# Kernel tuning notes

Hardware: AMD Instinct MI355X
Metric: run time of the kernel (lower is better)

Reference implementation:

```python
import jax, jax.numpy as jnp
import numpy as np

LEAK = 0.2
N = 1024      # nodes
C_IN = 64     # input channels
C_OUT = 64    # output channels
L = 2         # num_degrees -> L**2 = 4 spherical-harmonic index
LSQ = L * L
T = 15        # num_eret (edge retyping)


def setup_inputs() -> dict:
    key = jax.random.key(0)
    k1, k2, k3, k4 = jax.random.split(key, 4)
    x = jax.random.normal(k1, (N, C_IN), dtype=jnp.float32)
    adjacency = jax.random.normal(k2, (N, N, LSQ, T), dtype=jnp.float32)
    # learned params (truncated_normal init in keras; plain normal*0.05 here)
    W = jax.random.normal(k3, (C_IN, C_OUT, LSQ, T), dtype=jnp.float32) * 0.05
    W2 = jax.random.normal(k4, (C_IN, C_OUT), dtype=jnp.float32) * 0.05
    return {"x": x, "adjacency": adjacency, "W": W, "W2": W2}


def reference(x, adjacency, W, W2):
    # adjacency-weighted spherical-harmonic message passing:
    # temp[m, j] = sum_{n,i,l,t} adj[m,n,l,t] * x[n,i] * W[i,j,l,t]
    temp = jnp.einsum('mnlt,ni,ijlt->mj', adjacency, x, W)
    # skip / self connection
    temp = temp + jnp.einsum('ni,ij->nj', x, W2)
    # lrelu with leak 0.2 (use_bias=False)
    return jnp.maximum(temp, LEAK * temp)
```

## Files before the change

kernel.cpp:

```cpp
#include <hip/hip_runtime.h>
#include <hip/hip_bf16.h>
#include <stdint.h>

typedef __bf16 v8bf __attribute__((ext_vector_type(8)));
typedef float  v4f  __attribute__((ext_vector_type(4)));

#define LEAK 0.2f

static __device__ __forceinline__ unsigned short bf16rne(float f) {
    union { float f; uint32_t u; } v; v.f = f;
    return (unsigned short)((v.u + 0x7FFFu + ((v.u >> 16) & 1u)) >> 16);
}

static __device__ __forceinline__ void gload16(const void* g, void* l) {
    __builtin_amdgcn_global_load_lds(
        (const __attribute__((address_space(1))) void*)g,
        (__attribute__((address_space(3))) void*)l, 16, 0, 0);
}

__global__ __launch_bounds__(256) void k0_wt(const float* __restrict__ W,
                                             unsigned short* __restrict__ Wt) {
    __shared__ float tile[64][65];
    const int c0 = blockIdx.x * 64;
    const int t  = threadIdx.x;
    {
        const int cl = t & 63, ig = t >> 6;
#pragma unroll
        for (int r = 0; r < 16; ++r) {
            int i = ig + (r << 2);
            tile[i][cl] = W[i * 3840 + c0 + cl];
        }
    }
    __syncthreads();
    {
        const int il = t & 63, cg = t >> 6;
#pragma unroll
        for (int r = 0; r < 16; ++r) {
            int c = cg + (r << 2);
            Wt[(c0 + c) * 64 + il] = bf16rne(tile[il][c]);
        }
    }
}

__global__ __launch_bounds__(256) void k1_ygemm(const float* __restrict__ x,
                                                const unsigned short* __restrict__ Wt,
                                                unsigned short* __restrict__ Yt) {
    __shared__ unsigned short As[64 * 64];
    __shared__ unsigned short Bs[64 * 64];
    const int blk = blockIdx.x;
    const int nt = blk / 60, ct = blk % 60;
    const int n0 = nt * 64, c0 = ct * 64;
    const int t = threadIdx.x;
    char* const asb = (char*)As;
    char* const bsb = (char*)Bs;

#pragma unroll
    for (int r = 0; r < 4; ++r) {
        const int rr = (t >> 4) + (r << 4);
        const int cq = t & 15;
        const float4 v = *reinterpret_cast<const float4*>(x + (n0 + rr) * 64 + cq * 4);
        uint2 p;
        p.x = (uint32_t)bf16rne(v.x) | ((uint32_t)bf16rne(v.y) << 16);
        p.y = (uint32_t)bf16rne(v.z) | ((uint32_t)bf16rne(v.w) << 16);
        const int off = rr * 128 + ((cq * 8) ^ ((rr & 7) << 4));
        *reinterpret_cast<uint2*>(asb + off) = p;
    }
#pragma unroll
    for (int r = 0; r < 2; ++r) {
        const int chunk = t + (r << 8);
        const int row = chunk >> 3, c16 = chunk & 7;
        const uint4 v = *reinterpret_cast<const uint4*>(Wt + (c0 + row) * 64 + c16 * 8);
        const int off = row * 128 + ((c16 * 16) ^ ((row & 7) << 4));
        *reinterpret_cast<uint4*>(bsb + off) = v;
    }
    __syncthreads();

    const int w = t >> 6, l = t & 63;
    v4f acc[4];
#pragma unroll
    for (int jt = 0; jt < 4; ++jt) acc[jt] = (v4f){0.f, 0.f, 0.f, 0.f};

#pragma unroll
    for (int s = 0; s < 2; ++s) {
        const int ar = 16 * w + (l & 15);
        const v8bf af = *reinterpret_cast<const v8bf*>(
            asb + ar * 128 + ((64 * s + (l >> 4) * 16) ^ ((ar & 7) << 4)));
#pragma unroll
        for (int jt = 0; jt < 4; ++jt) {
            const int br = 16 * jt + (l & 15);
            const v8bf bf = *reinterpret_cast<const v8bf*>(
                bsb + br * 128 + ((64 * s + (l >> 4) * 16) ^ ((br & 7) << 4)));
            acc[jt] = __builtin_amdgcn_mfma_f32_16x16x32_bf16(af, bf, acc[jt], 0, 0, 0);
        }
    }

#pragma unroll
    for (int jt = 0; jt < 4; ++jt) {
#pragma unroll
        for (int r = 0; r < 4; ++r) {
            const int n = n0 + 16 * w + (l >> 4) * 4 + r;
            const int c = c0 + jt * 16 + (l & 15);
            const int j = c / 60, lt = c % 60;
            Yt[j * 61440 + n * 60 + lt] = bf16rne(acc[jt][r]);
        }
    }
}

__global__ __launch_bounds__(256) void k2_main(const float* __restrict__ adj,
                                               const unsigned short* __restrict__ Yt,
                                               float* __restrict__ partial) {
    __shared__ __align__(16) char lds[73728];
    const int blk = blockIdx.x;
    const int mt = blk >> 5, ks = blk & 31;
    const int m0 = mt * 64;
    const long kc0 = (long)ks * 1920;
    const int t = threadIdx.x;
    const int w = t >> 6, l = t & 63;
    const int lr = l & 15, lg = l >> 4;

    const char* srcA[4];
    const char* srcB[2];
#pragma unroll
    for (int k = 0; k < 4; ++k) {
        const int row = k * 16 + w * 4 + lg;
        srcA[k] = (const char*)(adj + (size_t)(m0 + row) * 61440 + kc0)
                  + ((lr * 16) ^ ((row & 7) << 4));
    }
#pragma unroll
    for (int k = 0; k < 2; ++k) {
        const int row = k * 32 + w * 8 + (l >> 3);
        srcB[k] = (const char*)(Yt + (size_t)row * 61440 + kc0)
                  + (((l & 7) * 16) ^ ((row & 7) << 4));
    }

#define STAGE(bs, s) do {                                                      \
        char* ab_ = lds + (bs) * 16384;                                        \
        char* bb_ = lds + 49152 + (bs) * 8192;                                 \
        _Pragma("unroll")                                                      \
        for (int k_ = 0; k_ < 4; ++k_)                                         \
            gload16(srcA[k_] + (size_t)(s) * 256, ab_ + k_ * 4096 + w * 1024); \
        _Pragma("unroll")                                                      \
        for (int k_ = 0; k_ < 2; ++k_)                                         \
            gload16(srcB[k_] + (size_t)(s) * 128, bb_ + k_ * 4096 + w * 1024); \
    } while (0)

    v4f acc[4];
#pragma unroll
    for (int jt = 0; jt < 4; ++jt) acc[jt] = (v4f){0.f, 0.f, 0.f, 0.f};

    const int ar = 16 * w + lr;
    const int sa = (ar & 7) << 4;

    STAGE(0, 0);
    STAGE(1, 1);
    int bs = 2, bc = 0;

#pragma unroll 1
    for (int i = 0; i < 30; ++i) {
        if (i < 29) { asm volatile("s_waitcnt vmcnt(6)" ::: "memory"); }
        else        { asm volatile("s_waitcnt vmcnt(0)" ::: "memory"); }
        __builtin_amdgcn_s_barrier();
        asm volatile("" ::: "memory");
        if (i < 28) STAGE(bs, i + 2);

        const char* ab = lds + bc * 16384;
        const char* bb = lds + 49152 + bc * 8192;
        v8bf af[2];
#pragma unroll
        for (int ss = 0; ss < 2; ++ss) {
            const int Xf = ss * 128 + lg * 32;
            const float4 x0 = *reinterpret_cast<const float4*>(ab + ar * 256 + (Xf ^ sa));
            const float4 x1 = *reinterpret_cast<const float4*>(ab + ar * 256 + ((Xf + 16) ^ sa));
            v8bf f;
            f[0] = (__bf16)x0.x; f[1] = (__bf16)x0.y;
            f[2] = (__bf16)x0.z; f[3] = (__bf16)x0.w;
            f[4] = (__bf16)x1.x; f[5] = (__bf16)x1.y;
            f[6] = (__bf16)x1.z; f[7] = (__bf16)x1.w;
            af[ss] = f;
        }
#pragma unroll
        for (int jt = 0; jt < 4; ++jt) {
            const int br = 16 * jt + lr;
            const int sb = (br & 7) << 4;
            const v8bf b0 = *reinterpret_cast<const v8bf*>(bb + br * 128 + ((lg * 16) ^ sb));
            const v8bf b1 = *reinterpret_cast<const v8bf*>(bb + br * 128 + ((64 + lg * 16) ^ sb));
            acc[jt] = __builtin_amdgcn_mfma_f32_16x16x32_bf16(af[0], b0, acc[jt], 0, 0, 0);
            acc[jt] = __builtin_amdgcn_mfma_f32_16x16x32_bf16(af[1], b1, acc[jt], 0, 0, 0);
        }

        bs = (bs == 2) ? 0 : bs + 1;
        bc = (bc == 2) ? 0 : bc + 1;
    }
#undef STAGE

    float* const p = partial + (long)ks * 65536;
#pragma unroll
    for (int jt = 0; jt < 4; ++jt) {
#pragma unroll
        for (int r = 0; r < 4; ++r) {
            const int m = m0 + 16 * w + lg * 4 + r;
            const int j = jt * 16 + lr;
            p[m * 64 + j] = acc[jt][r];
        }
    }
}

__global__ __launch_bounds__(256) void k3_epi(const float* __restrict__ partial,
                                              const float* __restrict__ x,
                                              const float* __restrict__ W2,
                                              float* __restrict__ out) {
    const int idx = blockIdx.x * 256 + threadIdx.x;
    const int m = idx >> 6, j = idx & 63;
    float s = 0.f;
#pragma unroll 8
    for (int sp = 0; sp < 32; ++sp) s += partial[sp * 65536 + idx];
    float sk = 0.f;
#pragma unroll 8
    for (int i = 0; i < 64; ++i) sk += x[m * 64 + i] * W2[i * 64 + j];
    const float v = s + sk;
    out[idx] = fmaxf(v, LEAK * v);
}

extern "C" void kernel_launch(void* const* d_in, const int* in_sizes, int n_in,
                              void* d_out, int out_size, void* d_ws, size_t ws_size,
                              hipStream_t stream) {
    const float* x   = (const float*)d_in[0];
    const float* adj = (const float*)d_in[1];
    const float* W   = (const float*)d_in[2];
    const float* W2  = (const float*)d_in[3];
    float* out = (float*)d_out;

    char* ws = (char*)d_ws;
    unsigned short* Wt = (unsigned short*)ws;
    unsigned short* Yt = (unsigned short*)(ws + 524288);
    float* partial     = (float*)(ws + 8388608);

    k0_wt   <<<60,  256, 0, stream>>>(W, Wt);
    k1_ygemm<<<960, 256, 0, stream>>>(x, Wt, Yt);
    k2_main <<<512, 256, 0, stream>>>(adj, Yt, partial);
    k3_epi  <<<256, 256, 0, stream>>>(partial, x, W2, out);
}
```

Baseline: 59.51 us.

## Fuse W transpose into Y GEMM and split-K reduction into main kernel

Removes the separate W transpose kernel by having the Y GEMM read fp32 W directly from global memory with strided loads and convert it in registers. Removes the epilogue kernel by having the last-arriving block per row tile, found with an atomic counter, reduce the split-K partials and apply the skip GEMM and leaky ReLU. Partials are now stored as bf16 to halve their traffic. This cuts launch count and partial traffic, at the cost of uncoalesced W reads, a memset, a serialized tail on the last block and lower precision in the reduction.

```diff
diff --git a/kernel.cpp b/kernel.cpp
--- a/kernel.cpp
+++ b/kernel.cpp
@@ -11,85 +11,46 @@
     union { float f; uint32_t u; } v; v.f = f;
     return (unsigned short)((v.u + 0x7FFFu + ((v.u >> 16) & 1u)) >> 16);
 }
-
+static __device__ __forceinline__ float bf2f(unsigned short s) {
+    union { uint32_t u; float f; } v; v.u = (uint32_t)s << 16; return v.f;
+}
 static __device__ __forceinline__ void gload16(const void* g, void* l) {
     __builtin_amdgcn_global_load_lds(
         (const __attribute__((address_space(1))) void*)g,
         (__attribute__((address_space(3))) void*)l, 16, 0, 0);
 }
 
-__global__ __launch_bounds__(256) void k0_wt(const float* __restrict__ W,
-                                             unsigned short* __restrict__ Wt) {
-    __shared__ float tile[64][65];
-    const int c0 = blockIdx.x * 64;
-    const int t  = threadIdx.x;
-    {
-        const int cl = t & 63, ig = t >> 6;
-#pragma unroll
-        for (int r = 0; r < 16; ++r) {
-            int i = ig + (r << 2);
-            tile[i][cl] = W[i * 3840 + c0 + cl];
-        }
-    }
-    __syncthreads();
-    {
-        const int il = t & 63, cg = t >> 6;
-#pragma unroll
-        for (int r = 0; r < 16; ++r) {
-            int c = cg + (r << 2);
-            Wt[(c0 + c) * 64 + il] = bf16rne(tile[il][c]);
-        }
-    }
-}
-
 __global__ __launch_bounds__(256) void k1_ygemm(const float* __restrict__ x,
-                                                const unsigned short* __restrict__ Wt,
+                                                const float* __restrict__ W,
                                                 unsigned short* __restrict__ Yt) {
-    __shared__ unsigned short As[64 * 64];
-    __shared__ unsigned short Bs[64 * 64];
     const int blk = blockIdx.x;
     const int nt = blk / 60, ct = blk % 60;
     const int n0 = nt * 64, c0 = ct * 64;
     const int t = threadIdx.x;
-    char* const asb = (char*)As;
-    char* const bsb = (char*)Bs;
-
-#pragma unroll
-    for (int r = 0; r < 4; ++r) {
-        const int rr = (t >> 4) + (r << 4);
-        const int cq = t & 15;
-        const float4 v = *reinterpret_cast<const float4*>(x + (n0 + rr) * 64 + cq * 4);
-        uint2 p;
-        p.x = (uint32_t)bf16rne(v.x) | ((uint32_t)bf16rne(v.y) << 16);
-        p.y = (uint32_t)bf16rne(v.z) | ((uint32_t)bf16rne(v.w) << 16);
-        const int off = rr * 128 + ((cq * 8) ^ ((rr & 7) << 4));
-        *reinterpret_cast<uint2*>(asb + off) = p;
-    }
-#pragma unroll
-    for (int r = 0; r < 2; ++r) {
-        const int chunk = t + (r << 8);
-        const int row = chunk >> 3, c16 = chunk & 7;
-        const uint4 v = *reinterpret_cast<const uint4*>(Wt + (c0 + row) * 64 + c16 * 8);
-        const int off = row * 128 + ((c16 * 16) ^ ((row & 7) << 4));
-        *reinterpret_cast<uint4*>(bsb + off) = v;
-    }
-    __syncthreads();
-
     const int w = t >> 6, l = t & 63;
+    const int lr = l & 15, lg = l >> 4;
+
     v4f acc[4];
 #pragma unroll
     for (int jt = 0; jt < 4; ++jt) acc[jt] = (v4f){0.f, 0.f, 0.f, 0.f};
 
+    const float* xr = x + (n0 + 16 * w + lr) * 64;
 #pragma unroll
     for (int s = 0; s < 2; ++s) {
-        const int ar = 16 * w + (l & 15);
-        const v8bf af = *reinterpret_cast<const v8bf*>(
-            asb + ar * 128 + ((64 * s + (l >> 4) * 16) ^ ((ar & 7) << 4)));
+        const float4 x0 = *reinterpret_cast<const float4*>(xr + s * 32 + lg * 8);
+        const float4 x1 = *reinterpret_cast<const float4*>(xr + s * 32 + lg * 8 + 4);
+        v8bf af;
+        af[0] = (__bf16)x0.x; af[1] = (__bf16)x0.y;
+        af[2] = (__bf16)x0.z; af[3] = (__bf16)x0.w;
+        af[4] = (__bf16)x1.x; af[5] = (__bf16)x1.y;
+        af[6] = (__bf16)x1.z; af[7] = (__bf16)x1.w;
+
+        const float* wb = W + (size_t)(s * 32 + lg * 8) * 3840 + c0 + lr;
 #pragma unroll
         for (int jt = 0; jt < 4; ++jt) {
-            const int br = 16 * jt + (l & 15);
-            const v8bf bf = *reinterpret_cast<const v8bf*>(
-                bsb + br * 128 + ((64 * s + (l >> 4) * 16) ^ ((br & 7) << 4)));
+            v8bf bf;
+#pragma unroll
+            for (int j = 0; j < 8; ++j) bf[j] = (__bf16)wb[(size_t)j * 3840 + jt * 16];
             acc[jt] = __builtin_amdgcn_mfma_f32_16x16x32_bf16(af, bf, acc[jt], 0, 0, 0);
         }
     }
@@ -98,8 +59,8 @@
     for (int jt = 0; jt < 4; ++jt) {
 #pragma unroll
         for (int r = 0; r < 4; ++r) {
-            const int n = n0 + 16 * w + (l >> 4) * 4 + r;
-            const int c = c0 + jt * 16 + (l & 15);
+            const int n = n0 + 16 * w + lg * 4 + r;
+            const int c = c0 + jt * 16 + lr;
             const int j = c / 60, lt = c % 60;
             Yt[j * 61440 + n * 60 + lt] = bf16rne(acc[jt][r]);
         }
@@ -108,8 +69,13 @@
 
 __global__ __launch_bounds__(256) void k2_main(const float* __restrict__ adj,
                                                const unsigned short* __restrict__ Yt,
-                                               float* __restrict__ partial) {
+                                               const float* __restrict__ x,
+                                               const float* __restrict__ W2,
+                                               unsigned short* __restrict__ partial,
+                                               int* __restrict__ cnt,
+                                               float* __restrict__ out) {
     __shared__ __align__(16) char lds[73728];
+    __shared__ int is_last;
     const int blk = blockIdx.x;
     const int mt = blk >> 5, ks = blk & 31;
     const int m0 = mt * 64;
@@ -193,32 +159,86 @@
     }
 #undef STAGE
 
-    float* const p = partial + (long)ks * 65536;
+    unsigned short* const p = partial + (size_t)ks * 65536;
 #pragma unroll
     for (int jt = 0; jt < 4; ++jt) {
 #pragma unroll
         for (int r = 0; r < 4; ++r) {
             const int m = m0 + 16 * w + lg * 4 + r;
             const int j = jt * 16 + lr;
-            p[m * 64 + j] = acc[jt][r];
-        }
-    }
-}
-
-__global__ __launch_bounds__(256) void k3_epi(const float* __restrict__ partial,
-                                              const float* __restrict__ x,
-                                              const float* __restrict__ W2,
-                                              float* __restrict__ out) {
-    const int idx = blockIdx.x * 256 + threadIdx.x;
-    const int m = idx >> 6, j = idx & 63;
-    float s = 0.f;
-#pragma unroll 8
-    for (int sp = 0; sp < 32; ++sp) s += partial[sp * 65536 + idx];
-    float sk = 0.f;
-#pragma unroll 8
-    for (int i = 0; i < 64; ++i) sk += x[m * 64 + i] * W2[i * 64 + j];
-    const float v = s + sk;
-    out[idx] = fmaxf(v, LEAK * v);
+            p[m * 64 + j] = bf16rne(acc[jt][r]);
+        }
+    }
+
+    __threadfence();
+    __syncthreads();
+    if (t == 0) {
+        const int old = __hip_atomic_fetch_add(cnt + mt, 1, __ATOMIC_ACQ_REL,
+                                               __HIP_MEMORY_SCOPE_AGENT);
+        is_last = (old == 31);
+    }
+    __syncthreads();
+    if (!is_last) return;
+    __threadfence();
+
+    const int ml = t >> 2;
+    const int j0 = (t & 3) * 16;
+    const int m = m0 + ml;
+
+    float accf[16];
+#pragma unroll
+    for (int e = 0; e < 16; ++e) accf[e] = 0.f;
+
+#pragma unroll 4
+    for (int sp = 0; sp < 32; ++sp) {
+        const unsigned short* pp = partial + (size_t)sp * 65536 + m * 64 + j0;
+        const uint4 a = *reinterpret_cast<const uint4*>(pp);
+        const uint4 b = *reinterpret_cast<const uint4*>(pp + 8);
+        accf[0]  += bf2f((unsigned short)(a.x & 0xffff));
+        accf[1]  += bf2f((unsigned short)(a.x >> 16));
+        accf[2]  += bf2f((unsigned short)(a.y & 0xffff));
+        accf[3]  += bf2f((unsigned short)(a.y >> 16));
+        accf[4]  += bf2f((unsigned short)(a.z & 0xffff));
+        accf[5]  += bf2f((unsigned short)(a.z >> 16));
+        accf[6]  += bf2f((unsigned short)(a.w & 0xffff));
+        accf[7]  += bf2f((unsigned short)(a.w >> 16));
+        accf[8]  += bf2f((unsigned short)(b.x & 0xffff));
+        accf[9]  += bf2f((unsigned short)(b.x >> 16));
+        accf[10] += bf2f((unsigned short)(b.y & 0xffff));
+        accf[11] += bf2f((unsigned short)(b.y >> 16));
+        accf[12] += bf2f((unsigned short)(b.z & 0xffff));
+        accf[13] += bf2f((unsigned short)(b.z >> 16));
+        accf[14] += bf2f((unsigned short)(b.w & 0xffff));
+        accf[15] += bf2f((unsigned short)(b.w >> 16));
+    }
+
+    const float* xrow = x + m * 64;
+#pragma unroll 4
+    for (int i = 0; i < 64; ++i) {
+        const float xv = xrow[i];
+        const float4 w0 = *reinterpret_cast<const float4*>(W2 + i * 64 + j0);
+        const float4 w1 = *reinterpret_cast<const float4*>(W2 + i * 64 + j0 + 4);
+        const float4 w2 = *reinterpret_cast<const float4*>(W2 + i * 64 + j0 + 8);
+        const float4 w3 = *reinterpret_cast<const float4*>(W2 + i * 64 + j0 + 12);
+        accf[0]  += xv * w0.x; accf[1]  += xv * w0.y;
+        accf[2]  += xv * w0.z; accf[3]  += xv * w0.w;
+        accf[4]  += xv * w1.x; accf[5]  += xv * w1.y;
+        accf[6]  += xv * w1.z; accf[7]  += xv * w1.w;
+        accf[8]  += xv * w2.x; accf[9]  += xv * w2.y;
+        accf[10] += xv * w2.z; accf[11] += xv * w2.w;
+        accf[12] += xv * w3.x; accf[13] += xv * w3.y;
+        accf[14] += xv * w3.z; accf[15] += xv * w3.w;
+    }
+
+#pragma unroll
+    for (int q = 0; q < 4; ++q) {
+        float4 o;
+        o.x = fmaxf(accf[q * 4 + 0], LEAK * accf[q * 4 + 0]);
+        o.y = fmaxf(accf[q * 4 + 1], LEAK * accf[q * 4 + 1]);
+        o.z = fmaxf(accf[q * 4 + 2], LEAK * accf[q * 4 + 2]);
+        o.w = fmaxf(accf[q * 4 + 3], LEAK * accf[q * 4 + 3]);
+        *reinterpret_cast<float4*>(out + m * 64 + j0 + q * 4) = o;
+    }
 }
 
 extern "C" void kernel_launch(void* const* d_in, const int* in_sizes, int n_in,
@@ -231,12 +251,11 @@
     float* out = (float*)d_out;
 
     char* ws = (char*)d_ws;
-    unsigned short* Wt = (unsigned short*)ws;
-    unsigned short* Yt = (unsigned short*)(ws + 524288);
-    float* partial     = (float*)(ws + 8388608);
-
-    k0_wt   <<<60,  256, 0, stream>>>(W, Wt);
-    k1_ygemm<<<960, 256, 0, stream>>>(x, Wt, Yt);
-    k2_main <<<512, 256, 0, stream>>>(adj, Yt, partial);
-    k3_epi  <<<256, 256, 0, stream>>>(partial, x, W2, out);
-}
+    unsigned short* Yt      = (unsigned short*)ws;
+    unsigned short* partial = (unsigned short*)(ws + 7864320);
+    int* cnt                = (int*)(ws + 12058624);
+
+    hipMemsetAsync(cnt, 0, 16 * sizeof(int), stream);
+    k1_ygemm<<<960, 256, 0, stream>>>(x, W, Yt);
+    k2_main <<<512, 256, 0, stream>>>(adj, Yt, x, W2, partial, cnt, out);
+}
```

Measured after the change: 158.7 us. +166.8%, slower.
